# Optimization experiments

Hardware: AMD Instinct MI355X
Metric: run time of the kernel (lower is better)

## Reference

```python
import jax, jax.numpy as jnp
import numpy as np

TN_LAYERS = 2
GCN_LAYERS = 2

def _gru(x, h0, Wih, Whh, bih, bhh):
    # x: (B,T,I), h0: (B,H) -> (B,T,H); torch nn.GRU gate math (r,z,n ordering)
    def step(h, xt):
        gi = xt @ Wih.T + bih
        gh = h @ Whh.T + bhh
        ir, iz, inn = jnp.split(gi, 3, axis=-1)
        hr, hz, hn = jnp.split(gh, 3, axis=-1)
        r = jax.nn.sigmoid(ir + hr)
        z = jax.nn.sigmoid(iz + hz)
        n = jnp.tanh(inn + r * hn)
        h_new = (1.0 - z) * n + z * h
        return h_new, h_new
    _, hs = jax.lax.scan(step, h0, jnp.swapaxes(x, 0, 1))
    return jnp.swapaxes(hs, 0, 1)

def _forward(x, x_mark, sp_emb, sp_W1, sp_b1, sp_W2, sp_b2, t_emb, t_Wih, t_Whh, t_bih, t_bhh,
             gcn_W, gcn_b, fr_W1, fr_b1, fr_W2, fr_b2, tr_Wih, tr_Whh, tr_bih, tr_bhh, out_W, out_b):
    B, T, N = x.shape
    L = sp_b1.shape[0]
    elu = jax.nn.elu
    # --- SpatialEncoder: (B,N,T) ++ static embed -> Linear,ELU,Linear -> (B,N,L)
    xs = jnp.swapaxes(x, 1, 2)
    xs = jnp.concatenate([xs, jnp.broadcast_to(sp_emb, (B,) + sp_emb.shape)], axis=-1)
    Xs = elu(xs @ sp_W1 + sp_b1) @ sp_W2 + sp_b2
    # --- TemporalEncoder: concat(x, x_mark, static time embed) -> GRU -> (B,T,L)
    xt = jnp.concatenate([x, x_mark, jnp.broadcast_to(t_emb, (B,) + t_emb.shape)], axis=-1)
    Xt = _gru(xt, jnp.zeros((B, L), x.dtype), t_Wih, t_Whh, t_bih, t_bhh)
    X = jnp.concatenate([Xs, Xt], axis=1)  # (B, N+T, L)
    # --- TN modules: dynamic adjacency tanh(relu(X X^T)) + weighted message passing.
    # The torch code extracts per-batch sparse edge lists from batch_adj and does
    # gather-weight-scatter over them; zero-weight edges contribute nothing, so this
    # equals dense weighted aggregation A @ X per batch.
    for ti in range(TN_LAYERS):
        A = jnp.tanh(jax.nn.relu(jnp.einsum('bnf,bmf->bnm', X, X)))  # (B,N+T,N+T)
        for li in range(GCN_LAYERS):
            X = elu(jnp.einsum('bnm,bmd->bnd', A, X) @ gcn_W[ti, li] + gcn_b[ti, li])
    # --- Rebuild branches
    Xs2, Xt2 = X[:, :N, :], X[:, N:, :]
    rs = elu(Xs2 @ fr_W1 + fr_b1) @ fr_W2 + fr_b2  # feature_rebuild: (B,N,T)
    rt = _gru(Xt2, jnp.zeros((B, N), x.dtype), tr_Wih, tr_Whh, tr_bih, tr_bhh)  # time_rebuild: (B,T,N)
    combined = rs + jnp.swapaxes(rt, 1, 2)  # (B,N,T)
    return combined @ out_W + out_b  # (B, N, out_seq_len)

def setup_inputs():
    key = jax.random.key(0)
    B, T, N, Dt, L, E = 8, 96, 2000, 4, 32, 32
    ks = iter(jax.random.split(key, 32))
    nrm = lambda shape, s: jax.random.normal(next(ks), shape, jnp.float32) * s
    return {
        'x': nrm((B, T, N), 1.0),
        'x_mark': nrm((B, T, Dt), 1.0),
        'sp_emb': nrm((N, E), 0.1),
        'sp_W1': nrm((T + E, L), (T + E) ** -0.5), 'sp_b1': jnp.zeros((L,), jnp.float32),
        'sp_W2': nrm((L, L), L ** -0.5), 'sp_b2': jnp.zeros((L,), jnp.float32),
        't_emb': nrm((T, E), 0.1),
        't_Wih': nrm((3 * L, N + Dt + E), (N + Dt + E) ** -0.5),
        't_Whh': nrm((3 * L, L), L ** -0.5),
        't_bih': jnp.zeros((3 * L,), jnp.float32), 't_bhh': jnp.zeros((3 * L,), jnp.float32),
        'gcn_W': nrm((TN_LAYERS, GCN_LAYERS, L, L), 3e-3),  # small scale: dense aggregation sums ~N+T terms
        'gcn_b': jnp.zeros((TN_LAYERS, GCN_LAYERS, L), jnp.float32),
        'fr_W1': nrm((L, T), L ** -0.5), 'fr_b1': jnp.zeros((T,), jnp.float32),
        'fr_W2': nrm((T, T), T ** -0.5), 'fr_b2': jnp.zeros((T,), jnp.float32),
        'tr_Wih': nrm((3 * N, L), L ** -0.5), 'tr_Whh': nrm((3 * N, N), N ** -0.5),
        'tr_bih': jnp.zeros((3 * N,), jnp.float32), 'tr_bhh': jnp.zeros((3 * N,), jnp.float32),
        'out_W': nrm((T, 1), T ** -0.5), 'out_b': jnp.zeros((1,), jnp.float32),
    }

def reference(x, x_mark, sp_emb, sp_W1, sp_b1, sp_W2, sp_b2, t_emb, t_Wih, t_Whh, t_bih, t_bhh,
              gcn_W, gcn_b, fr_W1, fr_b1, fr_W2, fr_b2, tr_Wih, tr_Whh, tr_bih, tr_bhh, out_W, out_b):
    return _forward(x, x_mark, sp_emb, sp_W1, sp_b1, sp_W2, sp_b2, t_emb, t_Wih, t_Whh, t_bih, t_bhh,
                    gcn_W, gcn_b, fr_W1, fr_b1, fr_W2, fr_b2, tr_Wih, tr_Whh, tr_bih, tr_bhh, out_W, out_b)
```

## Files before the change

kernel.cpp:

```cpp
#include <hip/hip_runtime.h>

typedef _Float16 half8 __attribute__((ext_vector_type(8)));
typedef float f32x4 __attribute__((ext_vector_type(4)));

#define NBLK 125
#define TOTBLK 250
#define BAR_INTS (TOTBLK * 32)

__global__ __launch_bounds__(256) void k_pre(
    const float* __restrict__ x, const float* __restrict__ x_mark,
    const float* __restrict__ sp_emb,
    const float* __restrict__ spW1, const float* __restrict__ spb1,
    const float* __restrict__ spW2, const float* __restrict__ spb2,
    const float* __restrict__ t_emb, const float* __restrict__ tWih,
    const float* __restrict__ tbih,
    _Float16* __restrict__ X, float* __restrict__ gi,
    int* __restrict__ seq, unsigned char* __restrict__ hA) {
  __shared__ __align__(16) unsigned char PSM[65152];
  int tid = threadIdx.x;
  if (blockIdx.x < 63) {
    float* W1s = (float*)PSM;
    float* W2s = (float*)(PSM + 16384);
    float* b1s = (float*)(PSM + 20480);
    float* b2s = (float*)(PSM + 20608);
    int gidx = blockIdx.x * 256 + tid;
    for (int i = gidx; i < BAR_INTS; i += 63 * 256) seq[i] = 0;
    for (int i = gidx; i < 4000; i += 63 * 256) ((unsigned int*)hA)[i] = 0u;
    for (int i = tid; i < 128 * 32; i += 256) W1s[i] = spW1[i];
    for (int i = tid; i < 32 * 32; i += 256) W2s[i] = spW2[i];
    if (tid < 32) { b1s[tid] = spb1[tid]; b2s[tid] = spb2[tid]; }
    __syncthreads();
    if (gidx >= 8 * 2000) return;
    int b = gidx / 2000, n = gidx % 2000;
    float h1[32];
#pragma unroll
    for (int l = 0; l < 32; l++) h1[l] = b1s[l];
    for (int k = 0; k < 96; k++) {
      float xv = x[((size_t)b * 96 + k) * 2000 + n];
#pragma unroll
      for (int l = 0; l < 32; l++) h1[l] = fmaf(xv, W1s[k * 32 + l], h1[l]);
    }
    for (int e4 = 0; e4 < 8; e4++) {
      float4 ev = *reinterpret_cast<const float4*>(&sp_emb[(size_t)n * 32 + e4 * 4]);
      float evs[4] = {ev.x, ev.y, ev.z, ev.w};
#pragma unroll
      for (int q = 0; q < 4; q++) {
        int e = e4 * 4 + q;
#pragma unroll
        for (int l = 0; l < 32; l++) h1[l] = fmaf(evs[q], W1s[(96 + e) * 32 + l], h1[l]);
      }
    }
    float out[32];
#pragma unroll
    for (int j = 0; j < 32; j++) out[j] = b2s[j];
    for (int l = 0; l < 32; l++) {
      float a = h1[l] > 0.0f ? h1[l] : (__expf(h1[l]) - 1.0f);
#pragma unroll
      for (int j = 0; j < 32; j++) out[j] = fmaf(a, W2s[l * 32 + j], out[j]);
    }
    _Float16* dst = X + ((size_t)b * 2096 + n) * 32;
#pragma unroll
    for (int j8 = 0; j8 < 4; j8++) {
      half8 v;
#pragma unroll
      for (int q = 0; q < 8; q++) v[q] = (_Float16)out[j8 * 8 + q];
      *reinterpret_cast<half8*>(dst + j8 * 8) = v;
    }
  } else {
    float (*xs)[2036] = (float(*)[2036])PSM;
    int row0 = (blockIdx.x - 63) * 8;
    for (int rr = 0; rr < 8; rr++) {
      int row = row0 + rr;
      int b = row / 96, t = row % 96;
      for (int k = tid; k < 2036; k += 256) {
        float v;
        if (k < 2000) v = x[((size_t)b * 96 + t) * 2000 + k];
        else if (k < 2004) v = x_mark[((size_t)b * 96 + t) * 4 + (k - 2000)];
        else v = t_emb[(size_t)t * 32 + (k - 2004)];
        xs[rr][k] = v;
      }
    }
    __syncthreads();
    for (int oi = tid; oi < 8 * 96; oi += 256) {
      int rr = oi & 7, g = oi >> 3;
      const float* w = tWih + (size_t)g * 2036;
      float acc = tbih[g];
      for (int k = 0; k < 2036; k += 4) {
        float4 wv = *reinterpret_cast<const float4*>(w + k);
        acc = fmaf(xs[rr][k + 0], wv.x, acc);
        acc = fmaf(xs[rr][k + 1], wv.y, acc);
        acc = fmaf(xs[rr][k + 2], wv.z, acc);
        acc = fmaf(xs[rr][k + 3], wv.w, acc);
      }
      gi[(size_t)(row0 + rr) * 96 + g] = acc;
    }
  }
}

__global__ __launch_bounds__(768) void k_tgru(
    const float* __restrict__ gi, const float* __restrict__ Whh,
    const float* __restrict__ bhh, _Float16* __restrict__ X) {
  __shared__ float Whs[96][33];
  __shared__ float hs[8][33];
  __shared__ float ga[3][8][33];
  int tid = threadIdx.x;
  for (int i = tid; i < 96 * 32; i += 768) Whs[i >> 5][i & 31] = Whh[i];
  if (tid < 256) hs[tid >> 5][tid & 31] = 0.0f;
  int g = tid >> 8, j = (tid >> 3) & 31, b = tid & 7;
  int row = g * 32 + j;
  float bb0 = 0.f, bb1 = 0.f, bb2 = 0.f;
  if (tid < 256) {
    int jj = tid & 31;
    bb0 = bhh[jj]; bb1 = bhh[32 + jj]; bb2 = bhh[64 + jj];
  }
  __syncthreads();
  for (int t = 0; t < 96; t++) {
    float acc = 0.0f;
#pragma unroll
    for (int k = 0; k < 32; k++) acc = fmaf(hs[b][k], Whs[row][k], acc);
    ga[g][b][j] = acc;
    __syncthreads();
    if (tid < 256) {
      int bb = tid >> 5, jj = tid & 31;
      const float* gp = gi + ((size_t)bb * 96 + t) * 96;
      float gr = ga[0][bb][jj] + bb0;
      float gz = ga[1][bb][jj] + bb1;
      float gn = ga[2][bb][jj] + bb2;
      float r = 1.0f / (1.0f + __expf(-(gp[jj] + gr)));
      float z = 1.0f / (1.0f + __expf(-(gp[32 + jj] + gz)));
      float n = tanhf(gp[64 + jj] + r * gn);
      float hn = (1.0f - z) * n + z * hs[bb][jj];
      hs[bb][jj] = hn;
      X[((size_t)bb * 2096 + 2000 + t) * 32 + jj] = (_Float16)hn;
    }
    __syncthreads();
  }
}

__global__ __launch_bounds__(256) void k_gnn(
    const _Float16* __restrict__ Xa, const _Float16* __restrict__ Xin,
    _Float16* __restrict__ Xout, const float* __restrict__ W,
    const float* __restrict__ bias) {
  __shared__ _Float16 XaR[32][40];
  __shared__ _Float16 Xm[2][64][40];
  __shared__ _Float16 XqT[2][32][72];
  __shared__ _Float16 At[32][72];
  __shared__ float Pm[32][36];
  __shared__ float Ws[32][36];
  __shared__ float bs[32];
  int tid = threadIdx.x;
  int l = tid & 63, w = tid >> 6;
  int b = blockIdx.y;
  int r0 = blockIdx.x * 32;
  const _Float16* Xab = Xa + (size_t)b * 2096 * 32;
  const _Float16* Xib = Xin + (size_t)b * 2096 * 32;
  half8 hz = {(_Float16)0, (_Float16)0, (_Float16)0, (_Float16)0,
              (_Float16)0, (_Float16)0, (_Float16)0, (_Float16)0};

  for (int i = tid; i < 1024; i += 256) Ws[i >> 5][i & 31] = W[i];
  if (tid < 32) bs[tid] = bias[tid];
  if (tid < 128) {
    int r = tid >> 2, k = (tid & 3) * 8;
    half8 v = (r0 + r < 2096)
                  ? *reinterpret_cast<const half8*>(Xab + (size_t)(r0 + r) * 32 + k)
                  : hz;
    *reinterpret_cast<half8*>(&XaR[r][k]) = v;
  }
  int sr = tid >> 2, sk = (tid & 3) * 8;
  {
    *reinterpret_cast<half8*>(&Xm[0][sr][sk]) =
        *reinterpret_cast<const half8*>(Xab + (size_t)sr * 32 + sk);
    half8 vq = *reinterpret_cast<const half8*>(Xib + (size_t)sr * 32 + sk);
#pragma unroll
    for (int e = 0; e < 8; e++) XqT[0][sk + e][sr] = vq[e];
  }
  __syncthreads();

  int lr = l & 15, lk = (l >> 4) * 8, lq = (l >> 4) * 4;
  int smt = w >> 1, snt2 = w & 1;
  int pmt = w >> 1, pnt = w & 1;
  half8 afrag = *reinterpret_cast<const half8*>(&XaR[smt * 16 + lr][lk]);
  f32x4 pacc = {0.f, 0.f, 0.f, 0.f};

  for (int tt = 0; tt < 33; tt++) {
    int cur = tt & 1, nb = cur ^ 1;
    half8 vm = hz, vq = hz;
    bool hv = (tt + 1 < 33);
    if (hv) {
      int gm = (tt + 1) * 64 + sr;
      if (gm < 2096) {
        vm = *reinterpret_cast<const half8*>(Xab + (size_t)gm * 32 + sk);
        vq = *reinterpret_cast<const half8*>(Xib + (size_t)gm * 32 + sk);
      }
    }
#pragma unroll
    for (int n16 = 0; n16 < 2; n16++) {
      int c0 = snt2 * 32 + n16 * 16;
      half8 bfrag = *reinterpret_cast<const half8*>(&Xm[cur][c0 + lr][lk]);
      f32x4 s4 = __builtin_amdgcn_mfma_f32_16x16x32_f16(
          afrag, bfrag, (f32x4){0.f, 0.f, 0.f, 0.f}, 0, 0, 0);
#pragma unroll
      for (int j = 0; j < 4; j++) {
        float e = __expf(-2.0f * fmaxf(s4[j], 0.0f));
        At[smt * 16 + lq + j][c0 + lr] = (_Float16)((1.0f - e) / (1.0f + e));
      }
    }
    __syncthreads();
    {
      int nn = pnt * 16 + lr;
#pragma unroll
      for (int kc = 0; kc < 2; kc++) {
        half8 af = *reinterpret_cast<const half8*>(&At[pmt * 16 + lr][kc * 32 + lk]);
        half8 bf = *reinterpret_cast<const half8*>(&XqT[cur][nn][kc * 32 + lk]);
        pacc = __builtin_amdgcn_mfma_f32_16x16x32_f16(af, bf, pacc, 0, 0, 0);
      }
    }
    if (hv) {
      *reinterpret_cast<half8*>(&Xm[nb][sr][sk]) = vm;
#pragma unroll
      for (int e = 0; e < 8; e++) XqT[nb][sk + e][sr] = vq[e];
    }
    __syncthreads();
  }

#pragma unroll
  for (int j = 0; j < 4; j++) Pm[pmt * 16 + lq + j][pnt * 16 + lr] = pacc[j];
  __syncthreads();
  int r = tid & 31, fgr = tid >> 5;
  int f0 = fgr * 4;
  float o[4];
#pragma unroll
  for (int j = 0; j < 4; j++) o[j] = bs[f0 + j];
#pragma unroll
  for (int k = 0; k < 32; k++) {
    float mv = Pm[r][k];
    float4 wv = *reinterpret_cast<const float4*>(&Ws[k][f0]);
    o[0] = fmaf(mv, wv.x, o[0]);
    o[1] = fmaf(mv, wv.y, o[1]);
    o[2] = fmaf(mv, wv.z, o[2]);
    o[3] = fmaf(mv, wv.w, o[3]);
  }
  int grr = r0 + r;
  if (grr < 2096) {
    _Float16* dst = Xout + ((size_t)b * 2096 + grr) * 32 + f0;
#pragma unroll
    for (int j = 0; j < 4; j++) {
      float v = o[j];
      dst[j] = (_Float16)(v > 0.0f ? v : (__expf(v) - 1.0f));
    }
  }
}

__global__ __launch_bounds__(1024) void k_trgru(
    const _Float16* __restrict__ X, const float* __restrict__ wih,
    const float* __restrict__ bih, float* __restrict__ gi,
    const float* __restrict__ whh, const float* __restrict__ bhh,
    unsigned char* __restrict__ hA, unsigned char* __restrict__ hB,
    float* __restrict__ rt, int* __restrict__ seq,
    const float* __restrict__ frW1, const float* __restrict__ frb1,
    const float* __restrict__ frW2, const float* __restrict__ frb2,
    float* __restrict__ rs, const float* __restrict__ outW,
    const float* __restrict__ outb, float* __restrict__ out) {
  __shared__ __align__(16) unsigned char SM[122880];
  int tid = threadIdx.x;
  int blk = blockIdx.x;

  if (blk >= NBLK) {
    float* W1s = (float*)(SM);
    float* W2s = (float*)(SM + 12288);
    float* b1s = (float*)(SM + 50688);
    float* b2s = (float*)(SM + 51072);
    float* Xt  = (float*)(SM + 51456);
    float* Hl  = (float*)(SM + 55680);
    for (int i = tid; i < 32 * 96; i += 1024) W1s[i] = frW1[i];
    for (int i = tid; i < 96 * 96; i += 1024) W2s[(i / 96) * 100 + (i % 96)] = frW2[i];
    if (tid < 96) { b1s[tid] = frb1[tid]; b2s[tid] = frb2[tid]; }
    __syncthreads();
    for (int ti = blk - NBLK; ti < 504; ti += NBLK) {
      int b = ti / 63, n0 = (ti % 63) * 32;
      {
        int r = tid >> 5, k = tid & 31;
        Xt[r * 33 + k] =
            (n0 + r < 2000) ? (float)X[((size_t)b * 2096 + n0 + r) * 32 + k] : 0.0f;
      }
      __syncthreads();
#pragma unroll
      for (int q = 0; q < 3; q++) {
        int idx = q * 1024 + tid;
        int r = idx / 96, c = idx % 96;
        float a = b1s[c];
#pragma unroll 8
        for (int k = 0; k < 32; k++) a = fmaf(Xt[r * 33 + k], W1s[k * 96 + c], a);
        Hl[r * 100 + c] = a > 0.0f ? a : (__expf(a) - 1.0f);
      }
      __syncthreads();
#pragma unroll
      for (int q = 0; q < 3; q++) {
        int idx = q * 1024 + tid;
        int r = idx / 96, c = idx % 96;
        float o = b2s[c];
#pragma unroll 8
        for (int k = 0; k < 96; k++) o = fmaf(Hl[r * 100 + k], W2s[k * 100 + c], o);
        if (n0 + r < 2000) {
          __hip_atomic_store(&rs[((size_t)b * 2000 + n0 + r) * 96 + c], o,
                             __ATOMIC_RELAXED, __HIP_MEMORY_SCOPE_AGENT);
        }
      }
      __syncthreads();
    }
    if (tid == 0) {
      __hip_atomic_store(&seq[blk * 32], 96, __ATOMIC_RELAXED,
                         __HIP_MEMORY_SCOPE_AGENT);
    }
  } else {
    unsigned char* wf = SM;
    float* pt = (float*)(SM + 98304);
    int l = tid & 63, w = tid >> 6;

    for (int i = tid; i < 12288; i += 1024) ((unsigned long long*)wf)[i] = 0ull;

    if (tid < 768) {
      int t = tid >> 3, b = tid & 7;
      float xr[32];
      const _Float16* xp = X + ((size_t)b * 2096 + 2000 + t) * 32;
#pragma unroll
      for (int k = 0; k < 32; k++) xr[k] = (float)xp[k];
      float* gp = gi + ((size_t)b * 96 + t) * 6000;
      for (int g = 0; g < 3; g++) {
#pragma unroll
        for (int j = 0; j < 16; j++) {
          int row = g * 2000 + blk * 16 + j;
          const float* wr = wih + (size_t)row * 32;
          float a = bih[row];
#pragma unroll 8
          for (int k = 0; k < 32; k++) a = fmaf(xr[k], wr[k], a);
          gp[row] = a;
        }
      }
    }

    for (int i = tid; i < 3 * 64 * 64; i += 1024) {
      int g = i >> 12;
      int c = (i >> 6) & 63;
      int l2 = i & 63;
      int j = l2 & 15;
      int k0 = c * 32 + ((l2 >> 4) << 3);
      if (k0 <= 1992) {
        const float* src = whh + ((size_t)(g * 2000 + blk * 16 + j)) * 2000 + k0;
        float4 v0 = *reinterpret_cast<const float4*>(src);
        float4 v1 = *reinterpret_cast<const float4*>(src + 4);
        unsigned int lo = __builtin_amdgcn_cvt_pk_fp8_f32(v0.x, v0.y, 0, false);
        lo = __builtin_amdgcn_cvt_pk_fp8_f32(v0.z, v0.w, lo, true);
        unsigned int hi = __builtin_amdgcn_cvt_pk_fp8_f32(v1.x, v1.y, 0, false);
        hi = __builtin_amdgcn_cvt_pk_fp8_f32(v1.z, v1.w, hi, true);
        unsigned long long q = ((unsigned long long)hi << 32) | (unsigned long long)lo;
        *reinterpret_cast<unsigned long long*>(wf + (size_t)g * 32768 + c * 512 + l2 * 8) = q;
      }
    }

    int cj = tid >> 3, cb = tid & 7;
    int jg = blk * 16 + cj;
    float hold = 0.0f, bR = 0.f, bZ = 0.f, bN = 0.f;
    if (tid < 128) {
      bR = bhh[jg]; bZ = bhh[2000 + jg]; bN = bhh[4000 + jg];
    }
    int bb = l & 7, kblk = (l >> 4) * 8;
    __syncthreads();

    for (int t = 0; t < 96; t++) {
      const unsigned char* hc = (t & 1) ? hB : hA;
      unsigned char* hn = (t & 1) ? hA : hB;
      float gir = 0.f, giz = 0.f, gin = 0.f;
      if (tid < 128) {
        const float* gp = gi + ((size_t)cb * 96 + t) * 6000;
        gir = gp[jg]; giz = gp[2000 + jg]; gin = gp[4000 + jg];
      }
      f32x4 a0 = {0.f, 0.f, 0.f, 0.f}, a1 = {0.f, 0.f, 0.f, 0.f}, a2 = {0.f, 0.f, 0.f, 0.f};
#pragma unroll
      for (int i = 0; i < 4; i++) {
        int c = w * 4 + i;
        int k0 = c * 32 + kblk;
        long long bv = 0;
        if (k0 <= 1992)
          bv = *reinterpret_cast<const long long*>(hc + bb * 2000 + k0);
        long long w0 = *reinterpret_cast<const long long*>(wf + 0 * 32768 + c * 512 + l * 8);
        long long w1 = *reinterpret_cast<const long long*>(wf + 1 * 32768 + c * 512 + l * 8);
        long long w2 = *reinterpret_cast<const long long*>(wf + 2 * 32768 + c * 512 + l * 8);
        a0 = __builtin_amdgcn_mfma_f32_16x16x32_fp8_fp8(w0, bv, a0, 0, 0, 0);
        a1 = __builtin_amdgcn_mfma_f32_16x16x32_fp8_fp8(w1, bv, a1, 0, 0, 0);
        a2 = __builtin_amdgcn_mfma_f32_16x16x32_fp8_fp8(w2, bv, a2, 0, 0, 0);
      }
      {
        int bcol = l & 15;
        if (bcol < 8) {
          int lb = l >> 4;
          *reinterpret_cast<f32x4*>(pt + w * 384 + 0 * 128 + lb * 32 + bcol * 4) = a0;
          *reinterpret_cast<f32x4*>(pt + w * 384 + 1 * 128 + lb * 32 + bcol * 4) = a1;
          *reinterpret_cast<f32x4*>(pt + w * 384 + 2 * 128 + lb * 32 + bcol * 4) = a2;
        }
      }
      __syncthreads();
      if (tid < 128) {
        float s[3];
#pragma unroll
        for (int g = 0; g < 3; g++) {
          int base = g * 128 + (cj >> 2) * 32 + cb * 4 + (cj & 3);
          float acc = 0.f;
#pragma unroll
          for (int w2 = 0; w2 < 16; w2++) acc += pt[w2 * 384 + base];
          s[g] = acc;
        }
        float r_ = 1.0f / (1.0f + __expf(-(gir + s[0] + bR)));
        float z_ = 1.0f / (1.0f + __expf(-(giz + s[1] + bZ)));
        float n_ = tanhf(gin + r_ * (s[2] + bN));
        hold = (1.0f - z_) * n_ + z_ * hold;
        {
          unsigned int p = __builtin_amdgcn_cvt_pk_fp8_f32(hold, 0.0f, 0, false);
          __hip_atomic_store(hn + cb * 2000 + jg, (unsigned char)(p & 0xFF),
                             __ATOMIC_RELAXED, __HIP_MEMORY_SCOPE_AGENT);
        }
        __hip_atomic_store(&rt[((size_t)cb * 96 + t) * 2000 + jg], hold,
                           __ATOMIC_RELAXED, __HIP_MEMORY_SCOPE_AGENT);
      }
      __syncthreads();
      if (tid == 0) {
        __hip_atomic_store(&seq[blk * 32], t + 1, __ATOMIC_RELAXED,
                           __HIP_MEMORY_SCOPE_AGENT);
      }
      if ((tid >> 6) == 2) {
        int lane = tid & 63;
        const int* s1 = &seq[lane * 32];
        const int* s2 = &seq[((lane + 64) < NBLK ? (lane + 64) : lane) * 32];
        while (true) {
          int v1 = __hip_atomic_load(s1, __ATOMIC_RELAXED, __HIP_MEMORY_SCOPE_AGENT);
          int v2 = __hip_atomic_load(s2, __ATOMIC_RELAXED, __HIP_MEMORY_SCOPE_AGENT);
          if (__all(v1 > t && v2 > t)) break;
          __builtin_amdgcn_s_sleep(1);
        }
        if (lane == 0) {
          (void)__hip_atomic_load(s1, __ATOMIC_ACQUIRE, __HIP_MEMORY_SCOPE_AGENT);
        }
      }
      __syncthreads();
    }
  }

  {
    float* wsm = (float*)SM;
    __syncthreads();
    if (tid >= 128 && tid < 224) wsm[tid - 128] = outW[tid - 128];
    if (tid == 224) wsm[96] = outb[0];
    if (tid < 64) {
      const int* p0 = &seq[tid * 32];
      const int* p1 = &seq[(tid + 64) * 32];
      const int* p2 = &seq[(tid + 128) * 32];
      int i3 = tid + 192; if (i3 >= TOTBLK) i3 = tid;
      const int* p3 = &seq[i3 * 32];
      while (true) {
        int v0 = __hip_atomic_load(p0, __ATOMIC_RELAXED, __HIP_MEMORY_SCOPE_AGENT);
        int v1 = __hip_atomic_load(p1, __ATOMIC_RELAXED, __HIP_MEMORY_SCOPE_AGENT);
        int v2 = __hip_atomic_load(p2, __ATOMIC_RELAXED, __HIP_MEMORY_SCOPE_AGENT);
        int v3 = __hip_atomic_load(p3, __ATOMIC_RELAXED, __HIP_MEMORY_SCOPE_AGENT);
        if (__all(v0 >= 96 && v1 >= 96 && v2 >= 96 && v3 >= 96)) break;
        __builtin_amdgcn_s_sleep(2);
      }
      if (tid == 0) {
        (void)__hip_atomic_load(p0, __ATOMIC_ACQUIRE, __HIP_MEMORY_SCOPE_AGENT);
      }
    }
    __syncthreads();
    if (tid < 64) {
      int idx = blk * 64 + tid;
      int b = idx / 2000, n = idx % 2000;
      const float* rsp = rs + (size_t)idx * 96;
      float acc = wsm[96];
      for (int t4 = 0; t4 < 24; t4++) {
        float4 rv = *reinterpret_cast<const float4*>(rsp + t4 * 4);
        int t = t4 * 4;
        acc = fmaf(rv.x + rt[((size_t)b * 96 + t + 0) * 2000 + n], wsm[t + 0], acc);
        acc = fmaf(rv.y + rt[((size_t)b * 96 + t + 1) * 2000 + n], wsm[t + 1], acc);
        acc = fmaf(rv.z + rt[((size_t)b * 96 + t + 2) * 2000 + n], wsm[t + 2], acc);
        acc = fmaf(rv.w + rt[((size_t)b * 96 + t + 3) * 2000 + n], wsm[t + 3], acc);
      }
      out[idx] = acc;
    }
  }
}

extern "C" void kernel_launch(void* const* d_in, const int* in_sizes, int n_in,
                              void* d_out, int out_size, void* d_ws, size_t ws_size,
                              hipStream_t stream) {
  const float* x      = (const float*)d_in[0];
  const float* x_mark = (const float*)d_in[1];
  const float* sp_emb = (const float*)d_in[2];
  const float* sp_W1  = (const float*)d_in[3];
  const float* sp_b1  = (const float*)d_in[4];
  const float* sp_W2  = (const float*)d_in[5];
  const float* sp_b2  = (const float*)d_in[6];
  const float* t_emb  = (const float*)d_in[7];
  const float* t_Wih  = (const float*)d_in[8];
  const float* t_Whh  = (const float*)d_in[9];
  const float* t_bih  = (const float*)d_in[10];
  const float* t_bhh  = (const float*)d_in[11];
  const float* gcn_W  = (const float*)d_in[12];
  const float* gcn_b  = (const float*)d_in[13];
  const float* fr_W1  = (const float*)d_in[14];
  const float* fr_b1  = (const float*)d_in[15];
  const float* fr_W2  = (const float*)d_in[16];
  const float* fr_b2  = (const float*)d_in[17];
  const float* tr_Wih = (const float*)d_in[18];
  const float* tr_Whh = (const float*)d_in[19];
  const float* tr_bih = (const float*)d_in[20];
  const float* tr_bhh = (const float*)d_in[21];
  const float* out_W  = (const float*)d_in[22];
  const float* out_b  = (const float*)d_in[23];
  (void)in_sizes; (void)n_in; (void)out_size; (void)ws_size;

  float* ws = (float*)d_ws;
  float* X0   = ws;
  float* X1   = X0 + 536576;
  float* X2   = X1 + 536576;
  float* tgi  = X2 + 536576;
  float* trgi = tgi + 73728;
  float* hsl  = trgi + 4608000;
  float* rt   = hsl + 16000;
  float* rs   = rt + 1536000;
  float* barf = rs + 1536000;

  _Float16* X0h = (_Float16*)X0;
  _Float16* X1h = (_Float16*)X1;
  _Float16* X2h = (_Float16*)X2;
  unsigned char* hA = (unsigned char*)hsl;
  unsigned char* hB = hA + 16000;
  int* seq = (int*)barf;

  k_pre<<<159, 256, 0, stream>>>(x, x_mark, sp_emb, sp_W1, sp_b1, sp_W2, sp_b2,
                                 t_emb, t_Wih, t_bih, X0h, tgi, seq, hA);
  k_tgru<<<1, 768, 0, stream>>>(tgi, t_Whh, t_bhh, X0h);

  dim3 gg(66, 8);
  k_gnn<<<gg, 256, 0, stream>>>(X0h, X0h, X1h, gcn_W + 0 * 1024, gcn_b + 0 * 32);
  k_gnn<<<gg, 256, 0, stream>>>(X0h, X1h, X2h, gcn_W + 1 * 1024, gcn_b + 1 * 32);
  k_gnn<<<gg, 256, 0, stream>>>(X2h, X2h, X0h, gcn_W + 2 * 1024, gcn_b + 2 * 32);
  k_gnn<<<gg, 256, 0, stream>>>(X2h, X0h, X1h, gcn_W + 3 * 1024, gcn_b + 3 * 32);

  {
    const _Float16* a0 = X1h;
    const float* a1 = tr_Wih;
    const float* a2 = tr_bih;
    float* a3 = trgi;
    const float* a4 = tr_Whh;
    const float* a5 = tr_bhh;
    unsigned char* a6 = hA;
    unsigned char* a7 = hB;
    float* a8 = rt;
    int* a9 = seq;
    const float* a10 = fr_W1;
    const float* a11 = fr_b1;
    const float* a12 = fr_W2;
    const float* a13 = fr_b2;
    float* a14 = rs;
    const float* a15 = out_W;
    const float* a16 = out_b;
    float* a17 = (float*)d_out;
    void* cargs[] = {&a0, &a1, &a2, &a3, &a4, &a5, &a6, &a7, &a8, &a9,
                     &a10, &a11, &a12, &a13, &a14, &a15, &a16, &a17};
    hipLaunchCooperativeKernel((const void*)k_trgru, dim3(TOTBLK), dim3(1024), cargs, 0, stream);
  }
}
```

Before: 932.1 us.

## Fuse temporal GRU and four GNN layers into persistent cooperative mega-kernel

The separate temporal-GRU kernel, four GNN-layer launches and the time-rebuild cooperative kernel are merged into one persistent cooperative kernel. Block 0 runs the temporal GRU, and 132 blocks then each run four GNN tiles in parallel, one per 256-thread sub-group of a 1024-thread block. Grid-wide flag barriers separate the layers. This removes five kernel launches and their gaps, but it adds spin-wait barriers and gives each GNN tile fewer resident blocks per CU. The GRU stage is serial on one block while all other blocks wait.

Measured after the change: 1.055 ms. 13.2% more time.

```diff
diff --git a/kernel.cpp b/kernel.cpp
--- a/kernel.cpp
+++ b/kernel.cpp
@@ -5,7 +5,16 @@
 
 #define NBLK 125
 #define TOTBLK 250
-#define BAR_INTS (TOTBLK * 32)
+#define GNNBLK 132
+#define BAR_INTS 16000
+
+__device__ inline unsigned int pack2f16(float a, float b) {
+  _Float16 ha = (_Float16)a, hb = (_Float16)b;
+  unsigned short ua, ub;
+  __builtin_memcpy(&ua, &ha, 2);
+  __builtin_memcpy(&ub, &hb, 2);
+  return ((unsigned int)ub << 16) | ua;
+}
 
 __global__ __launch_bounds__(256) void k_pre(
     const float* __restrict__ x, const float* __restrict__ x_mark,
@@ -97,173 +106,225 @@
   }
 }
 
-__global__ __launch_bounds__(768) void k_tgru(
-    const float* __restrict__ gi, const float* __restrict__ Whh,
-    const float* __restrict__ bhh, _Float16* __restrict__ X) {
-  __shared__ float Whs[96][33];
-  __shared__ float hs[8][33];
-  __shared__ float ga[3][8][33];
-  int tid = threadIdx.x;
-  for (int i = tid; i < 96 * 32; i += 768) Whs[i >> 5][i & 31] = Whh[i];
-  if (tid < 256) hs[tid >> 5][tid & 31] = 0.0f;
-  int g = tid >> 8, j = (tid >> 3) & 31, b = tid & 7;
-  int row = g * 32 + j;
-  float bb0 = 0.f, bb1 = 0.f, bb2 = 0.f;
-  if (tid < 256) {
-    int jj = tid & 31;
-    bb0 = bhh[jj]; bb1 = bhh[32 + jj]; bb2 = bhh[64 + jj];
-  }
-  __syncthreads();
-  for (int t = 0; t < 96; t++) {
-    float acc = 0.0f;
-#pragma unroll
-    for (int k = 0; k < 32; k++) acc = fmaf(hs[b][k], Whs[row][k], acc);
-    ga[g][b][j] = acc;
-    __syncthreads();
-    if (tid < 256) {
-      int bb = tid >> 5, jj = tid & 31;
-      const float* gp = gi + ((size_t)bb * 96 + t) * 96;
-      float gr = ga[0][bb][jj] + bb0;
-      float gz = ga[1][bb][jj] + bb1;
-      float gn = ga[2][bb][jj] + bb2;
-      float r = 1.0f / (1.0f + __expf(-(gp[jj] + gr)));
-      float z = 1.0f / (1.0f + __expf(-(gp[32 + jj] + gz)));
-      float n = tanhf(gp[64 + jj] + r * gn);
-      float hn = (1.0f - z) * n + z * hs[bb][jj];
-      hs[bb][jj] = hn;
-      X[((size_t)bb * 2096 + 2000 + t) * 32 + jj] = (_Float16)hn;
-    }
-    __syncthreads();
-  }
-}
-
-__global__ __launch_bounds__(256) void k_gnn(
-    const _Float16* __restrict__ Xa, const _Float16* __restrict__ Xin,
-    _Float16* __restrict__ Xout, const float* __restrict__ W,
-    const float* __restrict__ bias) {
-  __shared__ _Float16 XaR[32][40];
-  __shared__ _Float16 Xm[2][64][40];
-  __shared__ _Float16 XqT[2][32][72];
-  __shared__ _Float16 At[32][72];
-  __shared__ float Pm[32][36];
-  __shared__ float Ws[32][36];
-  __shared__ float bs[32];
-  int tid = threadIdx.x;
-  int l = tid & 63, w = tid >> 6;
-  int b = blockIdx.y;
-  int r0 = blockIdx.x * 32;
-  const _Float16* Xab = Xa + (size_t)b * 2096 * 32;
-  const _Float16* Xib = Xin + (size_t)b * 2096 * 32;
-  half8 hz = {(_Float16)0, (_Float16)0, (_Float16)0, (_Float16)0,
-              (_Float16)0, (_Float16)0, (_Float16)0, (_Float16)0};
-
-  for (int i = tid; i < 1024; i += 256) Ws[i >> 5][i & 31] = W[i];
-  if (tid < 32) bs[tid] = bias[tid];
-  if (tid < 128) {
-    int r = tid >> 2, k = (tid & 3) * 8;
-    half8 v = (r0 + r < 2096)
-                  ? *reinterpret_cast<const half8*>(Xab + (size_t)(r0 + r) * 32 + k)
-                  : hz;
-    *reinterpret_cast<half8*>(&XaR[r][k]) = v;
-  }
-  int sr = tid >> 2, sk = (tid & 3) * 8;
-  {
-    *reinterpret_cast<half8*>(&Xm[0][sr][sk]) =
-        *reinterpret_cast<const half8*>(Xab + (size_t)sr * 32 + sk);
-    half8 vq = *reinterpret_cast<const half8*>(Xib + (size_t)sr * 32 + sk);
-#pragma unroll
-    for (int e = 0; e < 8; e++) XqT[0][sk + e][sr] = vq[e];
-  }
-  __syncthreads();
-
-  int lr = l & 15, lk = (l >> 4) * 8, lq = (l >> 4) * 4;
-  int smt = w >> 1, snt2 = w & 1;
-  int pmt = w >> 1, pnt = w & 1;
-  half8 afrag = *reinterpret_cast<const half8*>(&XaR[smt * 16 + lr][lk]);
-  f32x4 pacc = {0.f, 0.f, 0.f, 0.f};
-
-  for (int tt = 0; tt < 33; tt++) {
-    int cur = tt & 1, nb = cur ^ 1;
-    half8 vm = hz, vq = hz;
-    bool hv = (tt + 1 < 33);
-    if (hv) {
-      int gm = (tt + 1) * 64 + sr;
-      if (gm < 2096) {
-        vm = *reinterpret_cast<const half8*>(Xab + (size_t)gm * 32 + sk);
-        vq = *reinterpret_cast<const half8*>(Xib + (size_t)gm * 32 + sk);
-      }
-    }
-#pragma unroll
-    for (int n16 = 0; n16 < 2; n16++) {
-      int c0 = snt2 * 32 + n16 * 16;
-      half8 bfrag = *reinterpret_cast<const half8*>(&Xm[cur][c0 + lr][lk]);
-      f32x4 s4 = __builtin_amdgcn_mfma_f32_16x16x32_f16(
-          afrag, bfrag, (f32x4){0.f, 0.f, 0.f, 0.f}, 0, 0, 0);
-#pragma unroll
-      for (int j = 0; j < 4; j++) {
-        float e = __expf(-2.0f * fmaxf(s4[j], 0.0f));
-        At[smt * 16 + lq + j][c0 + lr] = (_Float16)((1.0f - e) / (1.0f + e));
-      }
-    }
-    __syncthreads();
-    {
-      int nn = pnt * 16 + lr;
-#pragma unroll
-      for (int kc = 0; kc < 2; kc++) {
-        half8 af = *reinterpret_cast<const half8*>(&At[pmt * 16 + lr][kc * 32 + lk]);
-        half8 bf = *reinterpret_cast<const half8*>(&XqT[cur][nn][kc * 32 + lk]);
-        pacc = __builtin_amdgcn_mfma_f32_16x16x32_f16(af, bf, pacc, 0, 0, 0);
-      }
-    }
-    if (hv) {
-      *reinterpret_cast<half8*>(&Xm[nb][sr][sk]) = vm;
-#pragma unroll
-      for (int e = 0; e < 8; e++) XqT[nb][sk + e][sr] = vq[e];
-    }
-    __syncthreads();
-  }
-
-#pragma unroll
-  for (int j = 0; j < 4; j++) Pm[pmt * 16 + lq + j][pnt * 16 + lr] = pacc[j];
-  __syncthreads();
-  int r = tid & 31, fgr = tid >> 5;
-  int f0 = fgr * 4;
-  float o[4];
-#pragma unroll
-  for (int j = 0; j < 4; j++) o[j] = bs[f0 + j];
-#pragma unroll
-  for (int k = 0; k < 32; k++) {
-    float mv = Pm[r][k];
-    float4 wv = *reinterpret_cast<const float4*>(&Ws[k][f0]);
-    o[0] = fmaf(mv, wv.x, o[0]);
-    o[1] = fmaf(mv, wv.y, o[1]);
-    o[2] = fmaf(mv, wv.z, o[2]);
-    o[3] = fmaf(mv, wv.w, o[3]);
-  }
-  int grr = r0 + r;
-  if (grr < 2096) {
-    _Float16* dst = Xout + ((size_t)b * 2096 + grr) * 32 + f0;
-#pragma unroll
-    for (int j = 0; j < 4; j++) {
-      float v = o[j];
-      dst[j] = (_Float16)(v > 0.0f ? v : (__expf(v) - 1.0f));
-    }
-  }
-}
-
-__global__ __launch_bounds__(1024) void k_trgru(
-    const _Float16* __restrict__ X, const float* __restrict__ wih,
-    const float* __restrict__ bih, float* __restrict__ gi,
-    const float* __restrict__ whh, const float* __restrict__ bhh,
-    unsigned char* __restrict__ hA, unsigned char* __restrict__ hB,
-    float* __restrict__ rt, int* __restrict__ seq,
+__global__ __launch_bounds__(1024) void k_mega(
+    _Float16* __restrict__ X0, _Float16* __restrict__ X1, _Float16* __restrict__ X2,
+    const float* __restrict__ tgi, const float* __restrict__ tWhh,
+    const float* __restrict__ tbhh,
+    const float* __restrict__ gcnW, const float* __restrict__ gcnb,
+    const float* __restrict__ wih, const float* __restrict__ bih,
+    float* __restrict__ gi, const float* __restrict__ whh,
+    const float* __restrict__ bhh, unsigned char* __restrict__ hA,
+    unsigned char* __restrict__ hB, float* __restrict__ rt,
+    int* __restrict__ seq,
     const float* __restrict__ frW1, const float* __restrict__ frb1,
     const float* __restrict__ frW2, const float* __restrict__ frb2,
     float* __restrict__ rs, const float* __restrict__ outW,
     const float* __restrict__ outb, float* __restrict__ out) {
-  __shared__ __align__(16) unsigned char SM[122880];
+  __shared__ __align__(16) unsigned char SM[147456];
   int tid = threadIdx.x;
   int blk = blockIdx.x;
+  int* gnnflags = seq + 8000;
+
+  if (blk == 0) {
+    float* Whs = (float*)SM;
+    float* hsb = (float*)(SM + 12672);
+    float* gab = (float*)(SM + 14016);
+    for (int i = tid; i < 96 * 32; i += 1024) Whs[(i >> 5) * 33 + (i & 31)] = tWhh[i];
+    if (tid < 256) hsb[(tid >> 5) * 33 + (tid & 31)] = 0.0f;
+    int g = tid >> 8, j = (tid >> 3) & 31, b = tid & 7;
+    int row = g * 32 + j;
+    float bb0 = 0.f, bb1 = 0.f, bb2 = 0.f;
+    if (tid < 256) {
+      int jj = tid & 31;
+      bb0 = tbhh[jj]; bb1 = tbhh[32 + jj]; bb2 = tbhh[64 + jj];
+    }
+    __syncthreads();
+    for (int t = 0; t < 96; t++) {
+      if (tid < 768) {
+        float acc = 0.0f;
+#pragma unroll
+        for (int k = 0; k < 32; k++) acc = fmaf(hsb[b * 33 + k], Whs[row * 33 + k], acc);
+        gab[(g * 8 + b) * 33 + j] = acc;
+      }
+      __syncthreads();
+      if (tid < 256) {
+        int bb = tid >> 5, jj = tid & 31;
+        const float* gp = tgi + ((size_t)bb * 96 + t) * 96;
+        float gr = gab[(0 * 8 + bb) * 33 + jj] + bb0;
+        float gz = gab[(1 * 8 + bb) * 33 + jj] + bb1;
+        float gn = gab[(2 * 8 + bb) * 33 + jj] + bb2;
+        float r = 1.0f / (1.0f + __expf(-(gp[jj] + gr)));
+        float z = 1.0f / (1.0f + __expf(-(gp[32 + jj] + gz)));
+        float n = tanhf(gp[64 + jj] + r * gn);
+        float hn2 = (1.0f - z) * n + z * hsb[bb * 33 + jj];
+        hsb[bb * 33 + jj] = hn2;
+        _Float16 hv = (_Float16)hn2;
+        unsigned short u;
+        __builtin_memcpy(&u, &hv, 2);
+        __hip_atomic_store((unsigned short*)(X0 + ((size_t)bb * 2096 + 2000 + t) * 32 + jj),
+                           u, __ATOMIC_RELAXED, __HIP_MEMORY_SCOPE_AGENT);
+      }
+      __syncthreads();
+    }
+  }
+  __syncthreads();
+  if (blk == 0 && tid == 0)
+    __hip_atomic_store(&gnnflags[0], 1, __ATOMIC_RELAXED, __HIP_MEMORY_SCOPE_AGENT);
+  if (tid == 0) {
+    while (__hip_atomic_load(&gnnflags[0], __ATOMIC_RELAXED, __HIP_MEMORY_SCOPE_AGENT) < 1)
+      __builtin_amdgcn_s_sleep(2);
+    (void)__hip_atomic_load(&gnnflags[0], __ATOMIC_ACQUIRE, __HIP_MEMORY_SCOPE_AGENT);
+  }
+  __syncthreads();
+
+  const _Float16* gXa[4] = {X0, X0, X2, X2};
+  const _Float16* gXi[4] = {X0, X1, X2, X0};
+  _Float16* gXo[4] = {X1, X2, X0, X1};
+  half8 hz = {(_Float16)0, (_Float16)0, (_Float16)0, (_Float16)0,
+              (_Float16)0, (_Float16)0, (_Float16)0, (_Float16)0};
+
+  for (int p = 0; p < 4; p++) {
+    if (blk < GNNBLK) {
+      int sub = tid >> 8, tid2 = tid & 255;
+      int unit = blk * 4 + sub;
+      int ub = unit / 66, ux = unit % 66;
+      int r0 = ux * 32;
+      _Float16* XaRp = (_Float16*)(SM + sub * 36864);
+      _Float16* Xmp  = XaRp + 1280;
+      _Float16* XqTp = Xmp + 5120;
+      _Float16* Atp  = XqTp + 4608;
+      float* Pmp = (float*)(Atp + 2304);
+      float* Wsp = Pmp + 1152;
+      float* bsp = Wsp + 1152;
+      const _Float16* Xab = gXa[p] + (size_t)ub * 2096 * 32;
+      const _Float16* Xib = gXi[p] + (size_t)ub * 2096 * 32;
+      _Float16* Xob = gXo[p] + (size_t)ub * 2096 * 32;
+      const float* W = gcnW + p * 1024;
+      const float* bias = gcnb + p * 32;
+
+      for (int i = tid2; i < 1024; i += 256) Wsp[(i >> 5) * 36 + (i & 31)] = W[i];
+      if (tid2 < 32) bsp[tid2] = bias[tid2];
+      if (tid2 < 128) {
+        int r = tid2 >> 2, k = (tid2 & 3) * 8;
+        half8 v = (r0 + r < 2096)
+                      ? *reinterpret_cast<const half8*>(Xab + (size_t)(r0 + r) * 32 + k)
+                      : hz;
+        *reinterpret_cast<half8*>(&XaRp[r * 40 + k]) = v;
+      }
+      int sr = tid2 >> 2, sk = (tid2 & 3) * 8;
+      {
+        *reinterpret_cast<half8*>(&Xmp[sr * 40 + sk]) =
+            *reinterpret_cast<const half8*>(Xab + (size_t)sr * 32 + sk);
+        half8 vq = *reinterpret_cast<const half8*>(Xib + (size_t)sr * 32 + sk);
+#pragma unroll
+        for (int e = 0; e < 8; e++) XqTp[(sk + e) * 72 + sr] = vq[e];
+      }
+      __syncthreads();
+
+      int l = tid2 & 63, w = tid2 >> 6;
+      int lr = l & 15, lk = (l >> 4) * 8, lq = (l >> 4) * 4;
+      int smt = w >> 1, snt2 = w & 1;
+      int pmt = w >> 1, pnt = w & 1;
+      half8 afrag = *reinterpret_cast<const half8*>(&XaRp[(smt * 16 + lr) * 40 + lk]);
+      f32x4 pacc = {0.f, 0.f, 0.f, 0.f};
+
+      for (int tt = 0; tt < 33; tt++) {
+        int cur = tt & 1, nb = cur ^ 1;
+        half8 vm = hz, vq = hz;
+        bool hv = (tt + 1 < 33);
+        if (hv) {
+          int gm = (tt + 1) * 64 + sr;
+          if (gm < 2096) {
+            vm = *reinterpret_cast<const half8*>(Xab + (size_t)gm * 32 + sk);
+            vq = *reinterpret_cast<const half8*>(Xib + (size_t)gm * 32 + sk);
+          }
+        }
+#pragma unroll
+        for (int n16 = 0; n16 < 2; n16++) {
+          int c0 = snt2 * 32 + n16 * 16;
+          half8 bfrag =
+              *reinterpret_cast<const half8*>(&Xmp[cur * 2560 + (c0 + lr) * 40 + lk]);
+          f32x4 s4 = __builtin_amdgcn_mfma_f32_16x16x32_f16(
+              afrag, bfrag, (f32x4){0.f, 0.f, 0.f, 0.f}, 0, 0, 0);
+#pragma unroll
+          for (int j = 0; j < 4; j++) {
+            float e = __expf(-2.0f * fmaxf(s4[j], 0.0f));
+            Atp[(smt * 16 + lq + j) * 72 + c0 + lr] =
+                (_Float16)((1.0f - e) / (1.0f + e));
+          }
+        }
+        __syncthreads();
+        {
+          int nn = pnt * 16 + lr;
+#pragma unroll
+          for (int kc = 0; kc < 2; kc++) {
+            half8 af = *reinterpret_cast<const half8*>(
+                &Atp[(pmt * 16 + lr) * 72 + kc * 32 + lk]);
+            half8 bf = *reinterpret_cast<const half8*>(
+                &XqTp[cur * 2304 + nn * 72 + kc * 32 + lk]);
+            pacc = __builtin_amdgcn_mfma_f32_16x16x32_f16(af, bf, pacc, 0, 0, 0);
+          }
+        }
+        if (hv) {
+          *reinterpret_cast<half8*>(&Xmp[nb * 2560 + sr * 40 + sk]) = vm;
+#pragma unroll
+          for (int e = 0; e < 8; e++) XqTp[nb * 2304 + (sk + e) * 72 + sr] = vq[e];
+        }
+        __syncthreads();
+      }
+
+#pragma unroll
+      for (int j = 0; j < 4; j++)
+        Pmp[(pmt * 16 + lq + j) * 36 + pnt * 16 + lr] = pacc[j];
+      __syncthreads();
+      int r = tid2 & 31, fgr = tid2 >> 5;
+      int f0 = fgr * 4;
+      float o[4];
+#pragma unroll
+      for (int j = 0; j < 4; j++) o[j] = bsp[f0 + j];
+#pragma unroll
+      for (int k = 0; k < 32; k++) {
+        float mv = Pmp[r * 36 + k];
+        float4 wv = *reinterpret_cast<const float4*>(&Wsp[k * 36 + f0]);
+        o[0] = fmaf(mv, wv.x, o[0]);
+        o[1] = fmaf(mv, wv.y, o[1]);
+        o[2] = fmaf(mv, wv.z, o[2]);
+        o[3] = fmaf(mv, wv.w, o[3]);
+      }
+      int grr = r0 + r;
+      if (grr < 2096) {
+#pragma unroll
+        for (int j = 0; j < 4; j++) {
+          float v = o[j];
+          o[j] = v > 0.0f ? v : (__expf(v) - 1.0f);
+        }
+        unsigned int* dst = (unsigned int*)(Xob + ((size_t)grr) * 32 + f0);
+        __hip_atomic_store(dst, pack2f16(o[0], o[1]), __ATOMIC_RELAXED,
+                           __HIP_MEMORY_SCOPE_AGENT);
+        __hip_atomic_store(dst + 1, pack2f16(o[2], o[3]), __ATOMIC_RELAXED,
+                           __HIP_MEMORY_SCOPE_AGENT);
+      }
+    }
+    __syncthreads();
+    if (tid == 0)
+      __hip_atomic_store(&gnnflags[blk * 32], p + 2, __ATOMIC_RELAXED,
+                         __HIP_MEMORY_SCOPE_AGENT);
+    if (tid < 64) {
+      int i0 = tid, i1 = tid + 64, i2 = tid + 128, i3 = tid + 192;
+      if (i3 >= TOTBLK) i3 = tid;
+      while (true) {
+        int v0 = __hip_atomic_load(&gnnflags[i0 * 32], __ATOMIC_RELAXED, __HIP_MEMORY_SCOPE_AGENT);
+        int v1 = __hip_atomic_load(&gnnflags[i1 * 32], __ATOMIC_RELAXED, __HIP_MEMORY_SCOPE_AGENT);
+        int v2 = __hip_atomic_load(&gnnflags[i2 * 32], __ATOMIC_RELAXED, __HIP_MEMORY_SCOPE_AGENT);
+        int v3 = __hip_atomic_load(&gnnflags[i3 * 32], __ATOMIC_RELAXED, __HIP_MEMORY_SCOPE_AGENT);
+        if (__all(v0 >= p + 2 && v1 >= p + 2 && v2 >= p + 2 && v3 >= p + 2)) break;
+        __builtin_amdgcn_s_sleep(2);
+      }
+      if (tid == 0)
+        (void)__hip_atomic_load(&gnnflags[0], __ATOMIC_ACQUIRE, __HIP_MEMORY_SCOPE_AGENT);
+    }
+    __syncthreads();
+  }
 
   if (blk >= NBLK) {
     float* W1s = (float*)(SM);
@@ -281,7 +342,7 @@
       {
         int r = tid >> 5, k = tid & 31;
         Xt[r * 33 + k] =
-            (n0 + r < 2000) ? (float)X[((size_t)b * 2096 + n0 + r) * 32 + k] : 0.0f;
+            (n0 + r < 2000) ? (float)X1[((size_t)b * 2096 + n0 + r) * 32 + k] : 0.0f;
       }
       __syncthreads();
 #pragma unroll
@@ -322,7 +383,7 @@
     if (tid < 768) {
       int t = tid >> 3, b = tid & 7;
       float xr[32];
-      const _Float16* xp = X + ((size_t)b * 2096 + 2000 + t) * 32;
+      const _Float16* xp = X1 + ((size_t)b * 2096 + 2000 + t) * 32;
 #pragma unroll
       for (int k = 0; k < 32; k++) xr[k] = (float)xp[k];
       float* gp = gi + ((size_t)b * 96 + t) * 6000;
@@ -536,35 +597,34 @@
 
   k_pre<<<159, 256, 0, stream>>>(x, x_mark, sp_emb, sp_W1, sp_b1, sp_W2, sp_b2,
                                  t_emb, t_Wih, t_bih, X0h, tgi, seq, hA);
-  k_tgru<<<1, 768, 0, stream>>>(tgi, t_Whh, t_bhh, X0h);
-
-  dim3 gg(66, 8);
-  k_gnn<<<gg, 256, 0, stream>>>(X0h, X0h, X1h, gcn_W + 0 * 1024, gcn_b + 0 * 32);
-  k_gnn<<<gg, 256, 0, stream>>>(X0h, X1h, X2h, gcn_W + 1 * 1024, gcn_b + 1 * 32);
-  k_gnn<<<gg, 256, 0, stream>>>(X2h, X2h, X0h, gcn_W + 2 * 1024, gcn_b + 2 * 32);
-  k_gnn<<<gg, 256, 0, stream>>>(X2h, X0h, X1h, gcn_W + 3 * 1024, gcn_b + 3 * 32);
 
   {
-    const _Float16* a0 = X1h;
-    const float* a1 = tr_Wih;
-    const float* a2 = tr_bih;
-    float* a3 = trgi;
-    const float* a4 = tr_Whh;
-    const float* a5 = tr_bhh;
-    unsigned char* a6 = hA;
-    unsigned char* a7 = hB;
-    float* a8 = rt;
-    int* a9 = seq;
-    const float* a10 = fr_W1;
-    const float* a11 = fr_b1;
-    const float* a12 = fr_W2;
-    const float* a13 = fr_b2;
-    float* a14 = rs;
-    const float* a15 = out_W;
-    const float* a16 = out_b;
-    float* a17 = (float*)d_out;
+    _Float16* a0 = X0h; _Float16* a1 = X1h; _Float16* a2 = X2h;
+    const float* a3 = tgi;
+    const float* a4 = t_Whh;
+    const float* a5 = t_bhh;
+    const float* a6 = gcn_W;
+    const float* a7 = gcn_b;
+    const float* a8 = tr_Wih;
+    const float* a9 = tr_bih;
+    float* a10 = trgi;
+    const float* a11 = tr_Whh;
+    const float* a12 = tr_bhh;
+    unsigned char* a13 = hA;
+    unsigned char* a14 = hB;
+    float* a15 = rt;
+    int* a16 = seq;
+    const float* a17 = fr_W1;
+    const float* a18 = fr_b1;
+    const float* a19 = fr_W2;
+    const float* a20 = fr_b2;
+    float* a21 = rs;
+    const float* a22 = out_W;
+    const float* a23 = out_b;
+    float* a24 = (float*)d_out;
     void* cargs[] = {&a0, &a1, &a2, &a3, &a4, &a5, &a6, &a7, &a8, &a9,
-                     &a10, &a11, &a12, &a13, &a14, &a15, &a16, &a17};
-    hipLaunchCooperativeKernel((const void*)k_trgru, dim3(TOTBLK), dim3(1024), cargs, 0, stream);
+                     &a10, &a11, &a12, &a13, &a14, &a15, &a16, &a17, &a18, &a19,
+                     &a20, &a21, &a22, &a23, &a24};
+    hipLaunchCooperativeKernel((const void*)k_mega, dim3(TOTBLK), dim3(1024), cargs, 0, stream);
   }
 }
```
